# Performance work log

Measured on AMD Instinct MI355X. Metric: run time of the kernel, lower is better.

## Reference

```python
import jax, jax.numpy as jnp
import numpy as np
from jax import lax

# Per-tensor power-of-two scales (ScalingImplType.CONST / POWER_OF_TWO in Brevitas)
S_ACT8 = 2.0 ** -4   # 8-bit signed input quant scale
S_ACT4 = 2.0 ** -1   # 4-bit signed input quant scale
S_W = 2.0 ** -2      # per-tensor weight quant scale
S_RELU = 2.0 ** -2   # 4-bit unsigned QuantReLU scale


def fq(x, scale, qmin, qmax):
    # fake-quant with straight-through estimator (STE)
    q = jnp.clip(jnp.round(x / scale), qmin, qmax) * scale
    return x + lax.stop_gradient(q - x)


def fq_signed(x, scale, bits):
    return fq(x, scale, -(2 ** (bits - 1)), 2 ** (bits - 1) - 1)


def fq_uint(x, scale, bits):
    return fq(x, scale, 0, 2 ** bits - 1)


def qconv(x, w, in_bits, w_bits, s_in, stride=1, padding=0, groups=1):
    xq = fq_signed(x, s_in, in_bits)
    wq = fq_signed(w, S_W, w_bits)
    return lax.conv_general_dilated(
        xq, wq, (stride, stride), [(padding, padding)] * 2,
        feature_group_count=groups,
        dimension_numbers=('NCHW', 'OIHW', 'NCHW'))


def maxpool(x, k, s):
    return lax.reduce_window(x, -jnp.inf, lax.max,
                             (1, 1, k, k), (1, 1, s, s), 'VALID')


def dwsep(x, dw, pw):
    c = x.shape[1]
    x = qconv(x, dw, 4, 4, S_ACT4, padding=1, groups=c)  # depthwise 3x3
    x = qconv(x, pw, 4, 4, S_ACT4)                       # pointwise 1x1
    return x


def qrelu4(x):
    return fq_uint(jax.nn.relu(x), S_RELU, 4)


def setup_inputs() -> dict:
    key = jax.random.key(0)
    ks = jax.random.split(key, 10)
    B = 1024
    mk = lambda k, shp, sc=0.5: jax.random.normal(k, shp, jnp.float32) * sc
    return {
        'x': jax.random.normal(ks[0], (B, 3, 32, 32), jnp.float32),
        'w0': mk(ks[1], (3, 3, 1, 1)),
        'dw1': mk(ks[2], (3, 1, 3, 3)),
        'pw1': mk(ks[3], (32, 3, 1, 1)),
        'dw2': mk(ks[4], (32, 1, 3, 3)),
        'pw2': mk(ks[5], (64, 32, 1, 1)),
        'dw3': mk(ks[6], (64, 1, 3, 3)),
        'pw3': mk(ks[7], (128, 64, 1, 1)),
        'wc1': mk(ks[8], (256, 128, 1, 1)),
        'wc2': mk(ks[9], (10, 256, 1, 1)),
    }


def reference(x, w0, dw1, pw1, dw2, pw2, dw3, pw3, wc1, wc2):
    # features
    h = qconv(x, w0, 8, 8, S_ACT8)            # 1x1, 3->3, 8-bit
    h = dwsep(h, dw1, pw1)                    # 3->32, 32x32
    h = qrelu4(h)
    h = maxpool(h, 2, 2)                      # 16x16
    h = dwsep(h, dw2, pw2)                    # 32->64
    h = qrelu4(h)
    h = maxpool(h, 2, 2)                      # 8x8
    h = dwsep(h, dw3, pw3)                    # 64->128
    h = qrelu4(h)
    h = maxpool(h, 8, 1)                      # 1x1
    # classifier
    h = qconv(h, wc1, 4, 4, S_ACT4)           # 128->256
    h = qrelu4(h)
    h = qconv(h, wc2, 4, 4, S_ACT4)           # 256->10
    h = fq_signed(h, S_ACT8, 8)               # output quant int8
    return h
```

## Files before the change

### kernel.cpp

```cpp
#include <hip/hip_runtime.h>

typedef int v4i __attribute__((ext_vector_type(4)));

#define W0i   0
#define DW1i  9
#define PW1i  36
#define DW2i  132
#define DW3i  420
#define PW2p  996
#define PW3p  1508
#define WC1p  3556
#define WC2p  11748
#define PW2Fb 12388
#define PW3Fb 12900
#define DW2pk 14948
#define DW3pk 15092
#define WTOT  15380

__device__ __forceinline__ int iclamp(int v, int lo, int hi) {
  return v < lo ? lo : (v > hi ? hi : v);
}
__device__ __forceinline__ int rne4(int a) {
  return (a + 1 + ((a >> 2) & 1)) >> 2;
}
__device__ __forceinline__ int rne32(int a) {
  return (a + 15 + ((a >> 5) & 1)) >> 5;
}

__device__ __forceinline__ void bar_lds() {
  asm volatile("s_waitcnt lgkmcnt(0)\n\ts_barrier" ::: "memory");
}

__device__ __forceinline__ int dot4(int a, int b, int c) {
#if defined(__has_builtin) && __has_builtin(__builtin_amdgcn_sdot4)
  return __builtin_amdgcn_sdot4(a, b, c, false);
#else
  c += ((a << 24) >> 24) * ((b << 24) >> 24);
  c += ((a << 16) >> 24) * ((b << 16) >> 24);
  c += ((a <<  8) >> 24) * ((b <<  8) >> 24);
  c += (a >> 24) * (b >> 24);
  return c;
#endif
}

__device__ __forceinline__ int alignb(int hi, int lo, int sh) {
#if defined(__has_builtin) && __has_builtin(__builtin_amdgcn_alignbyte)
  return __builtin_amdgcn_alignbyte(hi, lo, sh);
#else
  return (int)(((((unsigned long long)(unsigned)hi) << 32) |
                (unsigned)lo) >> (8 * sh));
#endif
}

__device__ __forceinline__ int pack3(int a, int b, int c) {
  return (a & 0xff) | ((b & 0xff) << 8) | ((c & 0xff) << 16);
}

__device__ __forceinline__ int pk_mad16(int a, int b, int c) {
  int d;
  asm("v_pk_mad_i16 %0, %1, %2, %3" : "=v"(d) : "v"(a), "v"(b), "v"(c));
  return d;
}
__device__ __forceinline__ int pk_add16(int a, int b) {
  int d;
  asm("v_pk_add_i16 %0, %1, %2" : "=v"(d) : "v"(a), "v"(b));
  return d;
}
__device__ __forceinline__ int pk_ashr16(int sh, int a) {
  int d;
  asm("v_pk_ashrrev_i16 %0, %1, %2" : "=v"(d) : "v"(sh), "v"(a));
  return d;
}
__device__ __forceinline__ int pk_max16(int a, int b) {
  int d;
  asm("v_pk_max_i16 %0, %1, %2" : "=v"(d) : "v"(a), "v"(b));
  return d;
}
__device__ __forceinline__ int pk_min16(int a, int b) {
  int d;
  asm("v_pk_min_i16 %0, %1, %2" : "=v"(d) : "v"(a), "v"(b));
  return d;
}
__device__ __forceinline__ int rne4s_pk(int a) {
  const int sh = 0x00020002, one = 0x00010001;
  int t = pk_ashr16(sh, a);
  t &= one;
  t += one;
  int s4 = pk_add16(a, t);
  int r = pk_ashr16(sh, s4);
  r = pk_max16(r, (int)0xFFF8FFF8);
  r = pk_min16(r, 0x00070007);
  return r;
}

__device__ __forceinline__ int max4(v4i d) {
  int a = d[0] > d[1] ? d[0] : d[1];
  int b = d[2] > d[3] ? d[2] : d[3];
  return a > b ? a : b;
}

__global__ __launch_bounds__(256) void prep_weights(
    const float* __restrict__ w0,  const float* __restrict__ dw1,
    const float* __restrict__ pw1, const float* __restrict__ dw2,
    const float* __restrict__ pw2, const float* __restrict__ dw3,
    const float* __restrict__ pw3, const float* __restrict__ wc1,
    const float* __restrict__ wc2, int* __restrict__ ws) {
  int t = blockIdx.x * blockDim.x + threadIdx.x;
  if (t >= WTOT) return;
  if (t < PW2p) {
    float w; int lo = -8, hi = 7;
    if (t < DW1i)      { w = w0[t];        lo = -128; hi = 127; }
    else if (t < PW1i)   w = dw1[t - DW1i];
    else if (t < DW2i)   w = pw1[t - PW1i];
    else if (t < DW3i)   w = dw2[t - DW2i];
    else                 w = dw3[t - DW3i];
    ws[t] = iclamp((int)rintf(w * 4.f), lo, hi);
  } else if (t < PW2Fb) {
    const float* src;
    if (t < WC1p) {
      if (t < PW3p) src = pw2 + (t - PW2p) * 4;
      else          src = pw3 + (t - PW3p) * 4;
    } else {
      if (t < WC2p) src = wc1 + (t - WC1p) * 4;
      else          src = wc2 + (t - WC2p) * 4;
    }
    int p = 0;
#pragma unroll
    for (int b = 0; b < 4; b++) {
      int c = iclamp((int)rintf(src[b] * 4.f), -8, 7);
      p |= (c & 0xff) << (8 * b);
    }
    ws[t] = p;
  } else if (t < PW3Fb) {
    int i = t - PW2Fb;
    int nt = i >> 7, r = i & 127, lane = r >> 1, dw = r & 1;
    int n = nt * 16 + (lane & 15);
    int kb = (lane >> 4) * 8 + dw * 4;
    int p = 0;
#pragma unroll
    for (int b = 0; b < 4; b++) {
      int c = iclamp((int)rintf(pw2[n * 32 + kb + b] * 4.f), -8, 7);
      p |= (c & 0xff) << (8 * b);
    }
    ws[t] = p;
  } else if (t < DW2pk) {
    int i = t - PW3Fb;
    int g = i >> 7, r = i & 127, lane = r >> 1, dw = r & 1;
    int nt = g >> 1, kh = g & 1;
    int n = nt * 16 + (lane & 15);
    int kb = kh * 32 + (lane >> 4) * 8 + dw * 4;
    int p = 0;
#pragma unroll
    for (int b = 0; b < 4; b++) {
      int c = iclamp((int)rintf(pw3[n * 64 + kb + b] * 4.f), -8, 7);
      p |= (c & 0xff) << (8 * b);
    }
    ws[t] = p;
  } else if (t < DW3pk) {
    int i = t - DW2pk;
    int cq = i / 18, r = i - cq * 18, t9 = r >> 1, par = r & 1;
    int wl = iclamp((int)rintf(dw2[(cq * 4 + par) * 9 + t9] * 4.f), -8, 7);
    int wh = iclamp((int)rintf(dw2[(cq * 4 + 2 + par) * 9 + t9] * 4.f), -8, 7);
    ws[t] = (wl & 0xFFFF) | (wh << 16);
  } else {
    int i = t - DW3pk;
    int cq = i / 18, r = i - cq * 18, t9 = r >> 1, par = r & 1;
    int wl = iclamp((int)rintf(dw3[(cq * 4 + par) * 9 + t9] * 4.f), -8, 7);
    int wh = iclamp((int)rintf(dw3[(cq * 4 + 2 + par) * 9 + t9] * 4.f), -8, 7);
    ws[t] = (wl & 0xFFFF) | (wh << 16);
  }
}

__global__ __launch_bounds__(256, 4) void fused_net(
    const float* __restrict__ x,
    const int*   __restrict__ wq,
    float* __restrict__ out)
{
  const int img = blockIdx.x;
  const int tid = threadIdx.x;
  const int wv = tid >> 6, lane = tid & 63;
  const int lm = lane & 15, kg = lane >> 4;

  __shared__ __align__(16) int bufAi[2560];
  __shared__ __align__(16) int bufBi[2592];

  const int ntp = (wv & 1) * 2;
  const long bw0 = *(const long*)(wq + PW2Fb + (ntp * 64 + lane) * 2);
  const long bw1 = *(const long*)(wq + PW2Fb + ((ntp + 1) * 64 + lane) * 2);
  long b0v[2], b1v[2];
#pragma unroll
  for (int h = 0; h < 2; h++) {
    int nt = wv * 2 + h;
    b0v[h] = *(const long*)(wq + PW3Fb + (nt * 2 + 0) * 128 + lane * 2);
    b1v[h] = *(const long*)(wq + PW3Fb + (nt * 2 + 1) * 128 + lane * 2);
  }

  {
    const float* xim = x + (size_t)img * 3072;
    const int p4 = tid * 4;
    float4 v0 = *(const float4*)(xim + p4);
    float4 v1 = *(const float4*)(xim + 1024 + p4);
    float4 v2 = *(const float4*)(xim + 2048 + p4);
    int w[9];
#pragma unroll
    for (int i = 0; i < 9; i++) w[i] = wq[W0i + i];
#define Q8(v) iclamp((int)rintf((v) * 16.f), -128, 127)
    int a0[4] = {Q8(v0.x), Q8(v0.y), Q8(v0.z), Q8(v0.w)};
    int a1[4] = {Q8(v1.x), Q8(v1.y), Q8(v1.z), Q8(v1.w)};
    int a2[4] = {Q8(v2.x), Q8(v2.y), Q8(v2.z), Q8(v2.w)};
#undef Q8
#pragma unroll
    for (int o = 0; o < 3; o++) {
      int pk = 0;
#pragma unroll
      for (int j = 0; j < 4; j++) {
        int s = a0[j] * w[o * 3] + a1[j] * w[o * 3 + 1] + a2[j] * w[o * 3 + 2];
        pk |= (iclamp(rne32(s), -8, 7) & 0xff) << (8 * j);
      }
      bufAi[o * 256 + tid] = pk;
    }
  }
  bar_lds();

  {
    const int y = tid >> 3, q = tid & 7;
#pragma unroll
    for (int c = 0; c < 3; c++) {
      int wr[3];
#pragma unroll
      for (int r = 0; r < 3; r++)
        wr[r] = pack3(wq[DW1i + c * 9 + r * 3], wq[DW1i + c * 9 + r * 3 + 1],
                      wq[DW1i + c * 9 + r * 3 + 2]);
      const int* ap = bufAi + c * 256;
      int acc0 = 0, acc1 = 0, acc2 = 0, acc3 = 0;
#pragma unroll
      for (int ky = 0; ky < 3; ky++) {
        int yy = y + ky - 1;
        if (yy < 0 || yy > 31) continue;
        int base = yy * 8 + q;
        int dC = ap[base];
        int dL = q ? ap[base - 1] : 0;
        int dR = (q < 7) ? ap[base + 1] : 0;
        int w = wr[ky];
        acc0 = dot4(alignb(dC, dL, 3), w, acc0);
        acc1 = dot4(dC, w, acc1);
        acc2 = dot4(alignb(dR, dC, 1), w, acc2);
        acc3 = dot4(alignb(dR, dC, 2), w, acc3);
      }
      int pk = (iclamp(rne4(acc0), -8, 7) & 0xff) |
               ((iclamp(rne4(acc1), -8, 7) & 0xff) << 8) |
               ((iclamp(rne4(acc2), -8, 7) & 0xff) << 16) |
               ((iclamp(rne4(acc3), -8, 7) & 0xff) << 24);
      bufBi[c * 256 + tid] = pk;
    }
  }
  bar_lds();

  {
    const int py = tid >> 4, px = tid & 15;
    const unsigned char* bB = (const unsigned char*)bufBi;
    unsigned u[3][2];
#pragma unroll
    for (int c = 0; c < 3; c++)
#pragma unroll
      for (int dy = 0; dy < 2; dy++)
        u[c][dy] = *(const unsigned short*)(bB + c * 1024 +
                                            (2 * py + dy) * 32 + 2 * px);
    int a[4];
#pragma unroll
    for (int d = 0; d < 4; d++) {
      int dy = d >> 1, dx = d & 1;
      unsigned t1 = __builtin_amdgcn_perm(u[1][dy], u[0][dy],
                                          0x0C0C0000u | ((4 + dx) << 8) | dx);
      a[d] = (int)__builtin_amdgcn_perm(u[2][dy], t1,
                                        0x0C000100u | ((4 + dx) << 16));
    }
#pragma unroll
    for (int it = 0; it < 8; it++) {
      int pk = 0;
#pragma unroll
      for (int j = 0; j < 4; j++) {
        int o = it * 4 + j;
        int wpk = pack3(wq[PW1i + o * 3], wq[PW1i + o * 3 + 1],
                        wq[PW1i + o * 3 + 2]);
        int m0 = dot4(a[0], wpk, 0), m1 = dot4(a[1], wpk, 0);
        int m2 = dot4(a[2], wpk, 0), m3 = dot4(a[3], wpk, 0);
        int mx = max(max(m0, m1), max(m2, m3));
        pk |= iclamp(rne4(mx), 0, 7) << (8 * j);
      }
      bufAi[py * 149 + px * 9 + it] = pk;
    }
  }
  bar_lds();

  for (int it2 = 0; it2 < 2; it2++) {
    int idx = tid + 256 * it2;
    int cq = __builtin_amdgcn_readfirstlane(idx >> 6);
    int s = idx & 63;
    int y = s >> 2, x0 = (s & 3) << 2;
    int we[9], wo[9];
    {
      const int2* wp = (const int2*)(wq + DW2pk + cq * 18);
#pragma unroll
      for (int t9 = 0; t9 < 9; t9++) { int2 v = wp[t9]; we[t9] = v.x; wo[t9] = v.y; }
    }
    int acce[4] = {}, acco[4] = {};
#pragma unroll
    for (int ky = 0; ky < 3; ky++) {
      int yy = y + ky - 1;
      if (yy < 0 || yy > 15) continue;
      int rb = yy * 149 + cq;
      int rd[6];
      rd[0] = (x0 > 0) ? bufAi[rb + (x0 - 1) * 9] : 0;
      rd[1] = bufAi[rb + x0 * 9];
      rd[2] = bufAi[rb + (x0 + 1) * 9];
      rd[3] = bufAi[rb + (x0 + 2) * 9];
      rd[4] = bufAi[rb + (x0 + 3) * 9];
      rd[5] = (x0 < 12) ? bufAi[rb + (x0 + 4) * 9] : 0;
      int ee[6], eo[6];
#pragma unroll
      for (int k = 0; k < 6; k++) {
        ee[k] = rd[k] & 0x000F000F;
        eo[k] = (rd[k] >> 8) & 0x000F000F;
      }
#pragma unroll
      for (int j = 0; j < 4; j++)
#pragma unroll
        for (int kx = 0; kx < 3; kx++) {
          acce[j] = pk_mad16(ee[j + kx], we[ky * 3 + kx], acce[j]);
          acco[j] = pk_mad16(eo[j + kx], wo[ky * 3 + kx], acco[j]);
        }
    }
    const int py = y >> 1, dy = y & 1;
#pragma unroll
    for (int j = 0; j < 4; j++) {
      int xx = x0 + j;
      int qp = py * 8 + (xx >> 1);
      int q = qp ^ (py & 3);
      int m = q * 4 + dy * 2 + (xx & 1);
      int re = rne4s_pk(acce[j]);
      int ro = rne4s_pk(acco[j]);
      bufBi[m * 10 + cq] = (re & 0x00FF00FF) | ((ro & 0x00FF00FF) << 8);
    }
  }
  bar_lds();

  {
    const int mtb = (wv >> 1) * 8;
    const signed char* Ab = (const signed char*)bufBi;
    signed char* A2c = (signed char*)bufAi;
    const int n0 = ntp * 16 + lm, n1 = (ntp + 1) * 16 + lm;
#pragma unroll 4
    for (int mt = mtb; mt < mtb + 8; mt++) {
      int m = mt * 16 + lm;
      long av = *(const long*)(Ab + m * 40 + kg * 8);
      v4i d0 = __builtin_amdgcn_mfma_i32_16x16x32_i8(av, bw0, (v4i){0, 0, 0, 0},
                                                     0, 0, 0);
      v4i d1 = __builtin_amdgcn_mfma_i32_16x16x32_i8(av, bw1, (v4i){0, 0, 0, 0},
                                                     0, 0, 0);
      int q = mt * 4 + kg;
      int qp = q ^ ((q >> 3) & 3);
      int py = qp >> 3, px = qp & 7;
      int bb = (py * 137 + px * 17) * 4;
      A2c[bb + n0] = (signed char)iclamp(rne4(max4(d0)), 0, 7);
      A2c[bb + n1] = (signed char)iclamp(rne4(max4(d1)), 0, 7);
    }
  }
  bar_lds();

  {
    int cq2 = tid >> 4;
    int s = tid & 15;
    int y = s >> 1, x0 = (s & 1) << 2;
    int we[9], wo[9];
    {
      const int2* wp = (const int2*)(wq + DW3pk + cq2 * 18);
#pragma unroll
      for (int t9 = 0; t9 < 9; t9++) { int2 v = wp[t9]; we[t9] = v.x; wo[t9] = v.y; }
    }
    int acce[4] = {}, acco[4] = {};
#pragma unroll
    for (int ky = 0; ky < 3; ky++) {
      int yy = y + ky - 1;
      if (yy < 0 || yy > 7) continue;
      int rb = yy * 137 + cq2;
      int rd[6];
      rd[0] = (x0 == 4) ? bufAi[rb + (x0 - 1) * 17] : 0;
      rd[1] = bufAi[rb + x0 * 17];
      rd[2] = bufAi[rb + (x0 + 1) * 17];
      rd[3] = bufAi[rb + (x0 + 2) * 17];
      rd[4] = bufAi[rb + (x0 + 3) * 17];
      rd[5] = (x0 == 0) ? bufAi[rb + (x0 + 4) * 17] : 0;
      int ee[6], eo[6];
#pragma unroll
      for (int k = 0; k < 6; k++) {
        ee[k] = rd[k] & 0x000F000F;
        eo[k] = (rd[k] >> 8) & 0x000F000F;
      }
#pragma unroll
      for (int j = 0; j < 4; j++)
#pragma unroll
        for (int kx = 0; kx < 3; kx++) {
          acce[j] = pk_mad16(ee[j + kx], we[ky * 3 + kx], acce[j]);
          acco[j] = pk_mad16(eo[j + kx], wo[ky * 3 + kx], acco[j]);
        }
    }
#pragma unroll
    for (int j = 0; j < 4; j++) {
      int re = rne4s_pk(acce[j]);
      int ro = rne4s_pk(acco[j]);
      bufBi[(y * 8 + x0 + j) * 18 + cq2] =
          (re & 0x00FF00FF) | ((ro & 0x00FF00FF) << 8);
    }
  }
  bar_lds();

  {
    const signed char* Ab = (const signed char*)bufBi;
    signed char* fcin = (signed char*)bufAi;
    int mx[2] = {-1000000, -1000000};
#pragma unroll
    for (int mt = 0; mt < 4; mt++) {
      int m = mt * 16 + lm;
      long a0 = *(const long*)(Ab + m * 72 + kg * 8);
      long a1 = *(const long*)(Ab + m * 72 + 32 + kg * 8);
#pragma unroll
      for (int h = 0; h < 2; h++) {
        v4i d = __builtin_amdgcn_mfma_i32_16x16x32_i8(a0, b0v[h],
                                                      (v4i){0, 0, 0, 0}, 0, 0, 0);
        d = __builtin_amdgcn_mfma_i32_16x16x32_i8(a1, b1v[h], d, 0, 0, 0);
        int t4 = max4(d);
        mx[h] = mx[h] > t4 ? mx[h] : t4;
      }
    }
#pragma unroll
    for (int h = 0; h < 2; h++) {
      int red = max(mx[h], __shfl_xor(mx[h], 16));
      red = max(red, __shfl_xor(red, 32));
      if (lane < 16)
        fcin[(wv * 2 + h) * 16 + lm] = (signed char)iclamp(rne4(red), 0, 7);
    }
  }
  bar_lds();

  {
    const int4* wp = (const int4*)(wq + WC1p + tid * 32);
    const int4* mp = (const int4*)bufAi;
    int acc = 0;
#pragma unroll
    for (int rI = 0; rI < 8; rI++) {
      int4 a = mp[rI]; int4 w = wp[rI];
      acc = dot4(a.x, w.x, acc); acc = dot4(a.y, w.y, acc);
      acc = dot4(a.z, w.z, acc); acc = dot4(a.w, w.w, acc);
    }
    ((signed char*)bufBi)[tid] = (signed char)iclamp(rne4(acc), 0, 7);
  }
  bar_lds();

  if (tid < 40) {
    int k = tid >> 2, j = tid & 3;
    const int4* wp = (const int4*)(wq + WC2p + k * 64 + j * 16);
    const int4* ap = (const int4*)bufBi;
    int acc = 0;
#pragma unroll
    for (int r = 0; r < 4; r++) {
      int4 a = ap[j * 4 + r]; int4 w = wp[r];
      acc = dot4(a.x, w.x, acc); acc = dot4(a.y, w.y, acc);
      acc = dot4(a.z, w.z, acc); acc = dot4(a.w, w.w, acc);
    }
    acc += __shfl_xor(acc, 1);
    acc += __shfl_xor(acc, 2);
    if (j == 0) {
      int code = iclamp(2 * acc, -128, 127);
      out[(size_t)img * 10 + k] = (float)code * 0.0625f;
    }
  }
}

extern "C" void kernel_launch(void* const* d_in, const int* in_sizes, int n_in,
                              void* d_out, int out_size, void* d_ws, size_t ws_size,
                              hipStream_t stream) {
  const float* x   = (const float*)d_in[0];
  const float* w0  = (const float*)d_in[1];
  const float* dw1 = (const float*)d_in[2];
  const float* pw1 = (const float*)d_in[3];
  const float* dw2 = (const float*)d_in[4];
  const float* pw2 = (const float*)d_in[5];
  const float* dw3 = (const float*)d_in[6];
  const float* pw3 = (const float*)d_in[7];
  const float* wc1 = (const float*)d_in[8];
  const float* wc2 = (const float*)d_in[9];
  int*   wsq = (int*)d_ws;
  float* out = (float*)d_out;

  prep_weights<<<(WTOT + 255) / 256, 256, 0, stream>>>(
      w0, dw1, pw1, dw2, pw2, dw3, pw3, wc1, wc2, wsq);
  fused_net<<<1024, 256, 0, stream>>>(x, wsq, out);
}
```

Measured before the change: 94.20 us.

## Fuse depthwise-1 into pointwise-1 stage, widen dw2 per-thread tile, prefetch FC weights

Each thread now computes the depthwise 3x3 for its own 2x2 pooling window straight from the quantized input rows held in LDS, then feeds the pointwise-1 and maxpool step directly. This removes one LDS round trip and one barrier, and the LDS buffer roles swap between stages to match. The dw2 stage now gives each thread 8 output columns instead of 4 over a single pass, so neighbouring loads are reused across more outputs. The first FC weights are loaded into registers before a barrier so the global-load latency can overlap. The cost is extra depthwise arithmetic, since neighbouring windows recompute overlapping rows, and higher register pressure.

```diff
diff --git a/kernel.cpp b/kernel.cpp
--- a/kernel.cpp
+++ b/kernel.cpp
@@ -223,57 +223,59 @@
   bar_lds();
 
   {
-    const int y = tid >> 3, q = tid & 7;
-#pragma unroll
-    for (int c = 0; c < 3; c++) {
-      int wr[3];
-#pragma unroll
-      for (int r = 0; r < 3; r++)
-        wr[r] = pack3(wq[DW1i + c * 9 + r * 3], wq[DW1i + c * 9 + r * 3 + 1],
-                      wq[DW1i + c * 9 + r * 3 + 2]);
-      const int* ap = bufAi + c * 256;
-      int acc0 = 0, acc1 = 0, acc2 = 0, acc3 = 0;
+    const int py = tid >> 4, px = tid & 15;
+    int wr[3][3], wrh[3][3];
+#pragma unroll
+    for (int c = 0; c < 3; c++)
 #pragma unroll
       for (int ky = 0; ky < 3; ky++) {
-        int yy = y + ky - 1;
-        if (yy < 0 || yy > 31) continue;
-        int base = yy * 8 + q;
-        int dC = ap[base];
-        int dL = q ? ap[base - 1] : 0;
-        int dR = (q < 7) ? ap[base + 1] : 0;
-        int w = wr[ky];
-        acc0 = dot4(alignb(dC, dL, 3), w, acc0);
-        acc1 = dot4(dC, w, acc1);
-        acc2 = dot4(alignb(dR, dC, 1), w, acc2);
-        acc3 = dot4(alignb(dR, dC, 2), w, acc3);
-      }
-      int pk = (iclamp(rne4(acc0), -8, 7) & 0xff) |
-               ((iclamp(rne4(acc1), -8, 7) & 0xff) << 8) |
-               ((iclamp(rne4(acc2), -8, 7) & 0xff) << 16) |
-               ((iclamp(rne4(acc3), -8, 7) & 0xff) << 24);
-      bufBi[c * 256 + tid] = pk;
-    }
-  }
-  bar_lds();
-
-  {
-    const int py = tid >> 4, px = tid & 15;
-    const unsigned char* bB = (const unsigned char*)bufBi;
-    unsigned u[3][2];
-#pragma unroll
-    for (int c = 0; c < 3; c++)
-#pragma unroll
-      for (int dy = 0; dy < 2; dy++)
-        u[c][dy] = *(const unsigned short*)(bB + c * 1024 +
-                                            (2 * py + dy) * 32 + 2 * px);
+        int w = pack3(wq[DW1i + c * 9 + ky * 3],
+                      wq[DW1i + c * 9 + ky * 3 + 1],
+                      wq[DW1i + c * 9 + ky * 3 + 2]);
+        wr[c][ky] = w;
+        wrh[c][ky] = w << 8;
+      }
+    const int s = (px & 1) ? 1 : 3;
+    const int D0 = (2 * px - 1) >> 2;
+    int V[3][4];
+#pragma unroll
+    for (int r = 0; r < 4; r++) {
+      int rr = 2 * py - 1 + r;
+      bool ok = (unsigned)rr < 32u;
+#pragma unroll
+      for (int c = 0; c < 3; c++) {
+        int lo = 0, hi = 0;
+        if (ok) {
+          const int* ap = bufAi + c * 256 + rr * 8;
+          if (px > 0)  lo = ap[D0];
+          if (px < 15) hi = ap[D0 + 1];
+        }
+        V[c][r] = alignb(hi, lo, s);
+      }
+    }
     int a[4];
 #pragma unroll
-    for (int d = 0; d < 4; d++) {
-      int dy = d >> 1, dx = d & 1;
-      unsigned t1 = __builtin_amdgcn_perm(u[1][dy], u[0][dy],
-                                          0x0C0C0000u | ((4 + dx) << 8) | dx);
-      a[d] = (int)__builtin_amdgcn_perm(u[2][dy], t1,
-                                        0x0C000100u | ((4 + dx) << 16));
+    for (int dy = 0; dy < 2; dy++) {
+      int r01[3];
+#pragma unroll
+      for (int c = 0; c < 3; c++) {
+        int acc0 = 0, acc1 = 0;
+#pragma unroll
+        for (int ky = 0; ky < 3; ky++) {
+          acc0 = dot4(V[c][dy + ky], wr[c][ky], acc0);
+          acc1 = dot4(V[c][dy + ky], wrh[c][ky], acc1);
+        }
+        int p = (int)__builtin_amdgcn_perm((unsigned)acc1, (unsigned)acc0,
+                                           0x05040100u);
+        r01[c] = rne4s_pk(p);
+      }
+      unsigned t0 = __builtin_amdgcn_perm((unsigned)r01[1], (unsigned)r01[0],
+                                          0x0C0C0400u);
+      a[2 * dy] = (int)__builtin_amdgcn_perm((unsigned)r01[2], t0, 0x0C040100u);
+      unsigned t1 = __builtin_amdgcn_perm((unsigned)r01[1], (unsigned)r01[0],
+                                          0x0C0C0602u);
+      a[2 * dy + 1] =
+          (int)__builtin_amdgcn_perm((unsigned)r01[2], t1, 0x0C060100u);
     }
 #pragma unroll
     for (int it = 0; it < 8; it++) {
@@ -288,43 +290,40 @@
         int mx = max(max(m0, m1), max(m2, m3));
         pk |= iclamp(rne4(mx), 0, 7) << (8 * j);
       }
-      bufAi[py * 149 + px * 9 + it] = pk;
-    }
-  }
-  bar_lds();
-
-  for (int it2 = 0; it2 < 2; it2++) {
-    int idx = tid + 256 * it2;
-    int cq = __builtin_amdgcn_readfirstlane(idx >> 6);
-    int s = idx & 63;
-    int y = s >> 2, x0 = (s & 3) << 2;
+      bufBi[py * 149 + px * 9 + it] = pk;
+    }
+  }
+  bar_lds();
+
+  {
+    const int cq = tid >> 5;
+    const int rem = tid & 31;
+    const int y = rem >> 1, xh = rem & 1, x0 = xh * 8;
     int we[9], wo[9];
     {
       const int2* wp = (const int2*)(wq + DW2pk + cq * 18);
 #pragma unroll
       for (int t9 = 0; t9 < 9; t9++) { int2 v = wp[t9]; we[t9] = v.x; wo[t9] = v.y; }
     }
-    int acce[4] = {}, acco[4] = {};
+    int acce[8] = {}, acco[8] = {};
 #pragma unroll
     for (int ky = 0; ky < 3; ky++) {
       int yy = y + ky - 1;
       if (yy < 0 || yy > 15) continue;
       int rb = yy * 149 + cq;
-      int rd[6];
-      rd[0] = (x0 > 0) ? bufAi[rb + (x0 - 1) * 9] : 0;
-      rd[1] = bufAi[rb + x0 * 9];
-      rd[2] = bufAi[rb + (x0 + 1) * 9];
-      rd[3] = bufAi[rb + (x0 + 2) * 9];
-      rd[4] = bufAi[rb + (x0 + 3) * 9];
-      rd[5] = (x0 < 12) ? bufAi[rb + (x0 + 4) * 9] : 0;
-      int ee[6], eo[6];
-#pragma unroll
-      for (int k = 0; k < 6; k++) {
+      int rd[10];
+      rd[0] = (x0 > 0) ? bufBi[rb + (x0 - 1) * 9] : 0;
+#pragma unroll
+      for (int k = 1; k < 9; k++) rd[k] = bufBi[rb + (x0 - 1 + k) * 9];
+      rd[9] = (x0 < 8) ? bufBi[rb + (x0 + 8) * 9] : 0;
+      int ee[10], eo[10];
+#pragma unroll
+      for (int k = 0; k < 10; k++) {
         ee[k] = rd[k] & 0x000F000F;
         eo[k] = (rd[k] >> 8) & 0x000F000F;
       }
 #pragma unroll
-      for (int j = 0; j < 4; j++)
+      for (int j = 0; j < 8; j++)
 #pragma unroll
         for (int kx = 0; kx < 3; kx++) {
           acce[j] = pk_mad16(ee[j + kx], we[ky * 3 + kx], acce[j]);
@@ -333,22 +332,22 @@
     }
     const int py = y >> 1, dy = y & 1;
 #pragma unroll
-    for (int j = 0; j < 4; j++) {
+    for (int j = 0; j < 8; j++) {
       int xx = x0 + j;
       int qp = py * 8 + (xx >> 1);
       int q = qp ^ (py & 3);
       int m = q * 4 + dy * 2 + (xx & 1);
       int re = rne4s_pk(acce[j]);
       int ro = rne4s_pk(acco[j]);
-      bufBi[m * 10 + cq] = (re & 0x00FF00FF) | ((ro & 0x00FF00FF) << 8);
+      bufAi[m * 10 + cq] = (re & 0x00FF00FF) | ((ro & 0x00FF00FF) << 8);
     }
   }
   bar_lds();
 
   {
     const int mtb = (wv >> 1) * 8;
-    const signed char* Ab = (const signed char*)bufBi;
-    signed char* A2c = (signed char*)bufAi;
+    const signed char* Ab = (const signed char*)bufAi;
+    signed char* A2c = (signed char*)bufBi;
     const int n0 = ntp * 16 + lm, n1 = (ntp + 1) * 16 + lm;
 #pragma unroll 4
     for (int mt = mtb; mt < mtb + 8; mt++) {
@@ -385,12 +384,12 @@
       if (yy < 0 || yy > 7) continue;
       int rb = yy * 137 + cq2;
       int rd[6];
-      rd[0] = (x0 == 4) ? bufAi[rb + (x0 - 1) * 17] : 0;
-      rd[1] = bufAi[rb + x0 * 17];
-      rd[2] = bufAi[rb + (x0 + 1) * 17];
-      rd[3] = bufAi[rb + (x0 + 2) * 17];
-      rd[4] = bufAi[rb + (x0 + 3) * 17];
-      rd[5] = (x0 == 0) ? bufAi[rb + (x0 + 4) * 17] : 0;
+      rd[0] = (x0 == 4) ? bufBi[rb + (x0 - 1) * 17] : 0;
+      rd[1] = bufBi[rb + x0 * 17];
+      rd[2] = bufBi[rb + (x0 + 1) * 17];
+      rd[3] = bufBi[rb + (x0 + 2) * 17];
+      rd[4] = bufBi[rb + (x0 + 3) * 17];
+      rd[5] = (x0 == 0) ? bufBi[rb + (x0 + 4) * 17] : 0;
       int ee[6], eo[6];
 #pragma unroll
       for (int k = 0; k < 6; k++) {
@@ -409,15 +408,21 @@
     for (int j = 0; j < 4; j++) {
       int re = rne4s_pk(acce[j]);
       int ro = rne4s_pk(acco[j]);
-      bufBi[(y * 8 + x0 + j) * 18 + cq2] =
+      bufAi[(y * 8 + x0 + j) * 18 + cq2] =
           (re & 0x00FF00FF) | ((ro & 0x00FF00FF) << 8);
     }
   }
-  bar_lds();
-
-  {
-    const signed char* Ab = (const signed char*)bufBi;
-    signed char* fcin = (signed char*)bufAi;
+  int4 wfc[8];
+  {
+    const int4* wp = (const int4*)(wq + WC1p + tid * 32);
+#pragma unroll
+    for (int rI = 0; rI < 8; rI++) wfc[rI] = wp[rI];
+  }
+  bar_lds();
+
+  {
+    const signed char* Ab = (const signed char*)bufAi;
+    signed char* fcin = (signed char*)bufBi;
     int mx[2] = {-1000000, -1000000};
 #pragma unroll
     for (int mt = 0; mt < 4; mt++) {
@@ -444,23 +449,22 @@
   bar_lds();
 
   {
-    const int4* wp = (const int4*)(wq + WC1p + tid * 32);
-    const int4* mp = (const int4*)bufAi;
+    const int4* mp = (const int4*)bufBi;
     int acc = 0;
 #pragma unroll
     for (int rI = 0; rI < 8; rI++) {
-      int4 a = mp[rI]; int4 w = wp[rI];
+      int4 a = mp[rI]; int4 w = wfc[rI];
       acc = dot4(a.x, w.x, acc); acc = dot4(a.y, w.y, acc);
       acc = dot4(a.z, w.z, acc); acc = dot4(a.w, w.w, acc);
     }
-    ((signed char*)bufBi)[tid] = (signed char)iclamp(rne4(acc), 0, 7);
+    ((signed char*)bufAi)[tid] = (signed char)iclamp(rne4(acc), 0, 7);
   }
   bar_lds();
 
   if (tid < 40) {
     int k = tid >> 2, j = tid & 3;
     const int4* wp = (const int4*)(wq + WC2p + k * 64 + j * 16);
-    const int4* ap = (const int4*)bufBi;
+    const int4* ap = (const int4*)bufAi;
     int acc = 0;
 #pragma unroll
     for (int r = 0; r < 4; r++) {
```

Result: no change. 93.07 us (-1.2%).
